# Performance work log

Measured on AMD Instinct MI355X. Metric: run time of the kernel, lower is better.

## Reference

```python
import jax, jax.numpy as jnp
import numpy as np

N_NODES = 50000
N_EDGES = 800000
D_IN, D_HID, D_OUT = 128, 128, 64


def setup_inputs() -> dict:
    key = jax.random.key(0)
    ks = jax.random.split(key, 10)
    return {
        "x": jax.random.normal(ks[0], (N_NODES, D_IN), dtype=jnp.float32),
        "edge_row": jax.random.randint(ks[1], (N_EDGES,), 0, N_NODES, dtype=jnp.int32),
        "edge_col": jax.random.randint(ks[2], (N_EDGES,), 0, N_NODES, dtype=jnp.int32),
        "edge_val": jax.random.uniform(ks[3], (N_EDGES,), dtype=jnp.float32),
        "W1": jax.random.normal(ks[4], (D_IN, D_HID), dtype=jnp.float32) * (1.0 / np.sqrt(D_HID)),
        "b1": jax.random.normal(ks[5], (D_HID,), dtype=jnp.float32) * (1.0 / np.sqrt(D_HID)),
        "W2": jax.random.normal(ks[6], (D_HID, D_HID), dtype=jnp.float32) * (1.0 / np.sqrt(D_HID)),
        "b2": jax.random.normal(ks[7], (D_HID,), dtype=jnp.float32) * (1.0 / np.sqrt(D_HID)),
        "W3": jax.random.normal(ks[8], (D_HID, D_OUT), dtype=jnp.float32) * (1.0 / np.sqrt(D_OUT)),
        "b3": jax.random.normal(ks[9], (D_OUT,), dtype=jnp.float32) * (1.0 / np.sqrt(D_OUT)),
    }


def _gcn_layer(x, edge_row, edge_col, edge_val, W, b):
    # support = x @ W          : dense GEMM [N, d_out]
    support = x @ W
    # spmm(adj, support)[i] = sum_e with row[e]==i: val[e] * support[col[e]]
    gathered = support[edge_col] * edge_val[:, None]  # [E, d_out]
    agg = jax.ops.segment_sum(gathered, edge_row, num_segments=x.shape[0])
    return agg + b


def reference(x, edge_row, edge_col, edge_val, W1, b1, W2, b2, W3, b3):
    # Layer 1 + ReLU (dropout is identity in eval)
    h = jax.nn.relu(_gcn_layer(x, edge_row, edge_col, edge_val, W1, b1))
    # Layer 2 + ReLU
    h = jax.nn.relu(_gcn_layer(h, edge_row, edge_col, edge_val, W2, b2))
    # Layer 3 (no activation)
    return _gcn_layer(h, edge_row, edge_col, edge_val, W3, b3)
```

## Files before the change

kernel.cpp:

```cpp
#include <hip/hip_runtime.h>

#define N_NODES 50000
#define N_EDGES 800000
#define SCAN_TILE 2048
#define CNT_STRIDE 16

static_assert(N_NODES < 65536, "col must fit in 16 bits for packed CSR");

typedef __attribute__((ext_vector_type(4))) float f32x4;
typedef __attribute__((ext_vector_type(8))) short bf16x8;

__device__ inline unsigned short f32_to_bf16(float f) {
    unsigned int u = __builtin_bit_cast(unsigned int, f);
    u += 0x7FFF + ((u >> 16) & 1);
    return (unsigned short)(u >> 16);
}
__device__ inline float bf16_to_f32(unsigned short h) {
    unsigned int u = ((unsigned int)h) << 16;
    return __builtin_bit_cast(float, u);
}

#define XN4   ((long long)N_NODES * 128 / 4)
#define W128  (128 * 128)
#define W64   (128 * 64)
#define CNT4  (N_NODES * CNT_STRIDE / 4)

__global__ void prep(const float* __restrict__ x, unsigned short* __restrict__ Xb,
                     const float* __restrict__ W1, const float* __restrict__ W2,
                     const float* __restrict__ W3, unsigned short* __restrict__ Wt1,
                     unsigned short* __restrict__ Wt2, unsigned short* __restrict__ Wt3,
                     int* __restrict__ cnt) {
    long long gid = (long long)blockIdx.x * blockDim.x + threadIdx.x;
    if (gid < XN4) {
        float4 v = reinterpret_cast<const float4*>(x)[gid];
        ushort4 o;
        o.x = f32_to_bf16(v.x); o.y = f32_to_bf16(v.y);
        o.z = f32_to_bf16(v.z); o.w = f32_to_bf16(v.w);
        reinterpret_cast<ushort4*>(Xb)[gid] = o;
        return;
    }
    long long r = gid - XN4;
    if (r < W128) {
        int k = (int)r / 128, m = (int)r % 128;
        Wt1[m * 128 + k] = f32_to_bf16(W1[r]);
        return;
    }
    r -= W128;
    if (r < W128) {
        int k = (int)r / 128, m = (int)r % 128;
        Wt2[m * 128 + k] = f32_to_bf16(W2[r]);
        return;
    }
    r -= W128;
    if (r < W64) {
        int k = (int)r / 64, m = (int)r % 64;
        Wt3[m * 128 + k] = f32_to_bf16(W3[r]);
        return;
    }
    r -= W64;
    if (r < CNT4) {
        int4 z = {0, 0, 0, 0};
        reinterpret_cast<int4*>(cnt)[r] = z;
    }
}

__global__ void rank_histogram(const int* __restrict__ erow, int* __restrict__ cnt,
                               int* __restrict__ rank) {
    int e = blockIdx.x * blockDim.x + threadIdx.x;
    if (e < N_EDGES) rank[e] = atomicAdd(&cnt[(size_t)erow[e] * CNT_STRIDE], 1);
}

__global__ void scan_tiles(const int* __restrict__ cnt, int* __restrict__ local,
                           int* __restrict__ tsum, int n) {
    __shared__ int sums[256];
    const int t = threadIdx.x;
    const int base = blockIdx.x * SCAN_TILE + t * 8;
    int v[8];
    int s = 0;
#pragma unroll
    for (int i = 0; i < 8; ++i) {
        v[i] = (base + i < n) ? cnt[(size_t)(base + i) * CNT_STRIDE] : 0;
        s += v[i];
    }
    sums[t] = s;
    __syncthreads();
    for (int off = 1; off < 256; off <<= 1) {
        int x = (t >= off) ? sums[t - off] : 0;
        __syncthreads();
        sums[t] += x;
        __syncthreads();
    }
    int run = sums[t] - s;
#pragma unroll
    for (int i = 0; i < 8; ++i) {
        if (base + i < n) local[base + i] = run;
        run += v[i];
    }
    if (t == 255) tsum[blockIdx.x] = run;
}

__global__ void scan_finalize(const int* __restrict__ local,
                              const int* __restrict__ tsum, int ntiles,
                              int* __restrict__ rptr, int n) {
    __shared__ int off_s;
    const int b = blockIdx.x;
    if (threadIdx.x == 0) {
        int s = 0;
        for (int i = 0; i < b; ++i) s += tsum[i];
        off_s = s;
        if (b == 0) {
            int tot = 0;
            for (int i = 0; i < ntiles; ++i) tot += tsum[i];
            rptr[n] = tot;
        }
    }
    __syncthreads();
    const int off = off_s;
    const int base = b * SCAN_TILE + threadIdx.x * 8;
#pragma unroll
    for (int i = 0; i < 8; ++i) {
        int idx = base + i;
        if (idx < n) rptr[idx] = local[idx] + off;
    }
}

__global__ void fill_csr(const int* __restrict__ erow, const int* __restrict__ ecol,
                         const float* __restrict__ eval, const int* __restrict__ rptr,
                         const int* __restrict__ rank,
                         unsigned int* __restrict__ cpack) {
    int e = blockIdx.x * blockDim.x + threadIdx.x;
    if (e >= N_EDGES) return;
    int slot = rptr[erow[e]] + rank[e];
    unsigned int p = (unsigned int)(ecol[e] & 0xFFFF) |
                     ((unsigned int)f32_to_bf16(eval[e]) << 16);
    cpack[slot] = p;
}

template <int NOUT, bool OUT_BF16>
__global__ __launch_bounds__(256) void gemm_mfma(
    const unsigned short* __restrict__ Xb, const unsigned short* __restrict__ Wt,
    void* __restrict__ Yv, int N, int ntiles) {
    constexpr int K = 128;
    constexpr int KP = K + 8;
    constexpr int NT = NOUT / 16;
    __shared__ unsigned short Xs[64 * KP];
    __shared__ unsigned short Ws[NOUT * KP];

    const int tid = threadIdx.x;
    const int wave = tid >> 6;
    const int lane = tid & 63;
    const int m = lane & 15;
    const int quad = lane >> 4;
    const int rowbase = wave * 16;

    for (int idx = tid; idx < NOUT * 16; idx += 256) {
        int r = idx >> 4, ch = idx & 15;
        uint4 v = *reinterpret_cast<const uint4*>(Wt + r * K + ch * 8);
        *reinterpret_cast<uint4*>(Ws + r * KP + ch * 8) = v;
    }

    for (int tile = blockIdx.x; tile < ntiles; tile += gridDim.x) {
        const int block_row = tile * 64;
        for (int idx = tid; idx < 64 * 16; idx += 256) {
            int r = idx >> 4, ch = idx & 15;
            int gr = block_row + r;
            if (gr >= N) gr = N - 1;
            uint4 v = *reinterpret_cast<const uint4*>(Xb + (size_t)gr * K + ch * 8);
            *reinterpret_cast<uint4*>(Xs + r * KP + ch * 8) = v;
        }
        __syncthreads();

        f32x4 acc[NT];
#pragma unroll
        for (int t = 0; t < NT; ++t) acc[t] = (f32x4){0.f, 0.f, 0.f, 0.f};

#pragma unroll
        for (int kt = 0; kt < 4; ++kt) {
            bf16x8 a = *reinterpret_cast<const bf16x8*>(
                Xs + (rowbase + m) * KP + kt * 32 + quad * 8);
#pragma unroll
            for (int t = 0; t < NT; ++t) {
                bf16x8 b = *reinterpret_cast<const bf16x8*>(
                    Ws + (t * 16 + m) * KP + kt * 32 + quad * 8);
                acc[t] = __builtin_amdgcn_mfma_f32_16x16x32_bf16(a, b, acc[t], 0, 0, 0);
            }
        }
        __syncthreads();

#pragma unroll
        for (int t = 0; t < NT; ++t) {
#pragma unroll
            for (int r = 0; r < 4; ++r) {
                int grow = block_row + rowbase + quad * 4 + r;
                if (grow < N) {
                    if (OUT_BF16)
                        reinterpret_cast<unsigned short*>(Yv)[(size_t)grow * NOUT + t * 16 + m] =
                            f32_to_bf16(acc[t][r]);
                    else
                        reinterpret_cast<float*>(Yv)[(size_t)grow * NOUT + t * 16 + m] = acc[t][r];
                }
            }
        }
    }
}

__global__ void aggregate_bf16(const unsigned short* __restrict__ S,
                               const int* __restrict__ rptr,
                               const unsigned int* __restrict__ cpack,
                               const float* __restrict__ bias,
                               unsigned short* __restrict__ outb, int N) {
    const int node = blockIdx.x * (blockDim.x / 16) + threadIdx.x / 16;
    const int f8 = threadIdx.x & 15;
    if (node >= N) return;
    const int beg = rptr[node];
    const int end = rptr[node + 1];
    float acc[8];
#pragma unroll
    for (int i = 0; i < 8; ++i) acc[i] = bias[f8 * 8 + i];
    int j = beg;
    for (; j + 8 <= end; j += 8) {
        unsigned int p[8];
        uint4 s[8];
#pragma unroll
        for (int u = 0; u < 8; ++u) p[u] = cpack[j + u];
#pragma unroll
        for (int u = 0; u < 8; ++u)
            s[u] = *reinterpret_cast<const uint4*>(S + (size_t)(p[u] & 0xFFFF) * 128 + f8 * 8);
#pragma unroll
        for (int u = 0; u < 8; ++u) {
            const float v = bf16_to_f32((unsigned short)(p[u] >> 16));
            const unsigned short* sp = reinterpret_cast<const unsigned short*>(&s[u]);
#pragma unroll
            for (int i = 0; i < 8; ++i) acc[i] = fmaf(v, bf16_to_f32(sp[i]), acc[i]);
        }
    }
    if (j + 4 <= end) {
        unsigned int p[4];
        uint4 s[4];
#pragma unroll
        for (int u = 0; u < 4; ++u) p[u] = cpack[j + u];
#pragma unroll
        for (int u = 0; u < 4; ++u)
            s[u] = *reinterpret_cast<const uint4*>(S + (size_t)(p[u] & 0xFFFF) * 128 + f8 * 8);
#pragma unroll
        for (int u = 0; u < 4; ++u) {
            const float v = bf16_to_f32((unsigned short)(p[u] >> 16));
            const unsigned short* sp = reinterpret_cast<const unsigned short*>(&s[u]);
#pragma unroll
            for (int i = 0; i < 8; ++i) acc[i] = fmaf(v, bf16_to_f32(sp[i]), acc[i]);
        }
        j += 4;
    }
    if (j + 2 <= end) {
        unsigned int p[2];
        uint4 s[2];
#pragma unroll
        for (int u = 0; u < 2; ++u) p[u] = cpack[j + u];
#pragma unroll
        for (int u = 0; u < 2; ++u)
            s[u] = *reinterpret_cast<const uint4*>(S + (size_t)(p[u] & 0xFFFF) * 128 + f8 * 8);
#pragma unroll
        for (int u = 0; u < 2; ++u) {
            const float v = bf16_to_f32((unsigned short)(p[u] >> 16));
            const unsigned short* sp = reinterpret_cast<const unsigned short*>(&s[u]);
#pragma unroll
            for (int i = 0; i < 8; ++i) acc[i] = fmaf(v, bf16_to_f32(sp[i]), acc[i]);
        }
        j += 2;
    }
    if (j < end) {
        unsigned int p = cpack[j];
        uint4 s = *reinterpret_cast<const uint4*>(S + (size_t)(p & 0xFFFF) * 128 + f8 * 8);
        const float v = bf16_to_f32((unsigned short)(p >> 16));
        const unsigned short* sp = reinterpret_cast<const unsigned short*>(&s);
#pragma unroll
        for (int i = 0; i < 8; ++i) acc[i] = fmaf(v, bf16_to_f32(sp[i]), acc[i]);
    }
    unsigned short o[8];
#pragma unroll
    for (int i = 0; i < 8; ++i) o[i] = f32_to_bf16(fmaxf(acc[i], 0.0f));
    *reinterpret_cast<uint4*>(outb + (size_t)node * 128 + f8 * 8) =
        *reinterpret_cast<uint4*>(o);
}

__global__ void aggregate_bf16_64(const unsigned short* __restrict__ S,
                                  const int* __restrict__ rptr,
                                  const unsigned int* __restrict__ cpack,
                                  const float* __restrict__ bias,
                                  float* __restrict__ out, int N) {
    const int node = blockIdx.x * (blockDim.x / 16) + threadIdx.x / 16;
    const int f4 = threadIdx.x & 15;
    if (node >= N) return;
    const int beg = rptr[node];
    const int end = rptr[node + 1];
    float acc[4];
#pragma unroll
    for (int i = 0; i < 4; ++i) acc[i] = bias[f4 * 4 + i];
    int j = beg;
    for (; j + 8 <= end; j += 8) {
        unsigned int p[8];
        uint2 s[8];
#pragma unroll
        for (int u = 0; u < 8; ++u) p[u] = cpack[j + u];
#pragma unroll
        for (int u = 0; u < 8; ++u)
            s[u] = *reinterpret_cast<const uint2*>(S + (size_t)(p[u] & 0xFFFF) * 64 + f4 * 4);
#pragma unroll
        for (int u = 0; u < 8; ++u) {
            const float v = bf16_to_f32((unsigned short)(p[u] >> 16));
            const unsigned short* sp = reinterpret_cast<const unsigned short*>(&s[u]);
#pragma unroll
            for (int i = 0; i < 4; ++i) acc[i] = fmaf(v, bf16_to_f32(sp[i]), acc[i]);
        }
    }
    if (j + 4 <= end) {
        unsigned int p[4];
        uint2 s[4];
#pragma unroll
        for (int u = 0; u < 4; ++u) p[u] = cpack[j + u];
#pragma unroll
        for (int u = 0; u < 4; ++u)
            s[u] = *reinterpret_cast<const uint2*>(S + (size_t)(p[u] & 0xFFFF) * 64 + f4 * 4);
#pragma unroll
        for (int u = 0; u < 4; ++u) {
            const float v = bf16_to_f32((unsigned short)(p[u] >> 16));
            const unsigned short* sp = reinterpret_cast<const unsigned short*>(&s[u]);
#pragma unroll
            for (int i = 0; i < 4; ++i) acc[i] = fmaf(v, bf16_to_f32(sp[i]), acc[i]);
        }
        j += 4;
    }
    if (j + 2 <= end) {
        unsigned int p[2];
        uint2 s[2];
#pragma unroll
        for (int u = 0; u < 2; ++u) p[u] = cpack[j + u];
#pragma unroll
        for (int u = 0; u < 2; ++u)
            s[u] = *reinterpret_cast<const uint2*>(S + (size_t)(p[u] & 0xFFFF) * 64 + f4 * 4);
#pragma unroll
        for (int u = 0; u < 2; ++u) {
            const float v = bf16_to_f32((unsigned short)(p[u] >> 16));
            const unsigned short* sp = reinterpret_cast<const unsigned short*>(&s[u]);
#pragma unroll
            for (int i = 0; i < 4; ++i) acc[i] = fmaf(v, bf16_to_f32(sp[i]), acc[i]);
        }
        j += 2;
    }
    if (j < end) {
        unsigned int p = cpack[j];
        uint2 s = *reinterpret_cast<const uint2*>(S + (size_t)(p & 0xFFFF) * 64 + f4 * 4);
        const float v = bf16_to_f32((unsigned short)(p >> 16));
        const unsigned short* sp = reinterpret_cast<const unsigned short*>(&s);
#pragma unroll
        for (int i = 0; i < 4; ++i) acc[i] = fmaf(v, bf16_to_f32(sp[i]), acc[i]);
    }
    float4 o = {acc[0], acc[1], acc[2], acc[3]};
    *reinterpret_cast<float4*>(out + (size_t)node * 64 + f4 * 4) = o;
}

extern "C" void kernel_launch(void* const* d_in, const int* in_sizes, int n_in,
                              void* d_out, int out_size, void* d_ws, size_t ws_size,
                              hipStream_t stream) {
    const float* x    = (const float*)d_in[0];
    const int*   erow = (const int*)d_in[1];
    const int*   ecol = (const int*)d_in[2];
    const float* eval = (const float*)d_in[3];
    const float* W1   = (const float*)d_in[4];
    const float* b1   = (const float*)d_in[5];
    const float* W2   = (const float*)d_in[6];
    const float* b2   = (const float*)d_in[7];
    const float* W3   = (const float*)d_in[8];
    const float* b3   = (const float*)d_in[9];
    float* out = (float*)d_out;

    const size_t nf = (size_t)N_NODES * 128;
    unsigned short* Xb  = (unsigned short*)d_ws;
    unsigned short* Ab  = Xb + nf;
    unsigned short* Wt1 = Ab + nf;
    unsigned short* Wt2 = Wt1 + 128 * 128;
    unsigned short* Wt3 = Wt2 + 128 * 128;
    int*   cnt    = (int*)(Wt3 + 64 * 128);
    int*   rank   = cnt + (size_t)N_NODES * CNT_STRIDE;
    int*   rptr   = rank + N_EDGES;
    unsigned int* cpack = (unsigned int*)(rptr + N_NODES + 1);
    int*   slocal = (int*)(cpack + N_EDGES);
    int*   stsum  = slocal + N_NODES;

    const int blk = 256;
    const int ntiles_g = (N_NODES + 63) / 64;
    const int gemm_grid = 256;
    const int agg_grid = (int)(((long long)N_NODES * 16 + blk - 1) / blk);
    const int ntiles = (N_NODES + SCAN_TILE - 1) / SCAN_TILE;

    {
        long long total = XN4 + W128 + W128 + W64 + CNT4;
        prep<<<(int)((total + blk - 1) / blk), blk, 0, stream>>>(
            x, Xb, W1, W2, W3, Wt1, Wt2, Wt3, cnt);
    }
    rank_histogram<<<(N_EDGES + blk - 1) / blk, blk, 0, stream>>>(erow, cnt, rank);
    scan_tiles<<<ntiles, 256, 0, stream>>>(cnt, slocal, stsum, N_NODES);
    scan_finalize<<<ntiles, 256, 0, stream>>>(slocal, stsum, ntiles, rptr, N_NODES);
    fill_csr<<<(N_EDGES + blk - 1) / blk, blk, 0, stream>>>(erow, ecol, eval, rptr,
                                                            rank, cpack);

    gemm_mfma<128, true><<<gemm_grid, 256, 0, stream>>>(Xb, Wt1, Ab, N_NODES, ntiles_g);
    aggregate_bf16<<<agg_grid, blk, 0, stream>>>(Ab, rptr, cpack, b1, Xb, N_NODES);

    gemm_mfma<128, true><<<gemm_grid, 256, 0, stream>>>(Xb, Wt2, Ab, N_NODES, ntiles_g);
    aggregate_bf16<<<agg_grid, blk, 0, stream>>>(Ab, rptr, cpack, b2, Xb, N_NODES);

    gemm_mfma<64, true><<<gemm_grid, 256, 0, stream>>>(Xb, Wt3, Ab, N_NODES, ntiles_g);
    aggregate_bf16_64<<<agg_grid, blk, 0, stream>>>(Ab, rptr, cpack, b3, out, N_NODES);
}
```

Measured before the change: 271.4 us.

## Fuse input conversion into GEMM1, merge scan kernels, overlap CSR fill with GEMM1

The first GEMM now reads the fp32 input directly and converts it to bf16 while staging into shared memory. This removes the separate pass that wrote and re-read a bf16 copy of x. The two scan kernels become one, with blocks coordinating through an atomic counter and spin-wait, which relies on all scan blocks being resident at once. The CSR fill runs as extra blocks inside the GEMM1 launch. Together these cut kernel launches and a full-size memory round trip.

```diff
diff --git a/kernel.cpp b/kernel.cpp
--- a/kernel.cpp
+++ b/kernel.cpp
@@ -4,6 +4,7 @@
 #define N_EDGES 800000
 #define SCAN_TILE 2048
 #define CNT_STRIDE 16
+#define GEMM_BLOCKS 256
 
 static_assert(N_NODES < 65536, "col must fit in 16 bits for packed CSR");
 
@@ -20,26 +21,16 @@
     return __builtin_bit_cast(float, u);
 }
 
-#define XN4   ((long long)N_NODES * 128 / 4)
 #define W128  (128 * 128)
 #define W64   (128 * 64)
 #define CNT4  (N_NODES * CNT_STRIDE / 4)
 
-__global__ void prep(const float* __restrict__ x, unsigned short* __restrict__ Xb,
-                     const float* __restrict__ W1, const float* __restrict__ W2,
+__global__ void prep(const float* __restrict__ W1, const float* __restrict__ W2,
                      const float* __restrict__ W3, unsigned short* __restrict__ Wt1,
                      unsigned short* __restrict__ Wt2, unsigned short* __restrict__ Wt3,
                      int* __restrict__ cnt) {
     long long gid = (long long)blockIdx.x * blockDim.x + threadIdx.x;
-    if (gid < XN4) {
-        float4 v = reinterpret_cast<const float4*>(x)[gid];
-        ushort4 o;
-        o.x = f32_to_bf16(v.x); o.y = f32_to_bf16(v.y);
-        o.z = f32_to_bf16(v.z); o.w = f32_to_bf16(v.w);
-        reinterpret_cast<ushort4*>(Xb)[gid] = o;
-        return;
-    }
-    long long r = gid - XN4;
+    long long r = gid;
     if (r < W128) {
         int k = (int)r / 128, m = (int)r % 128;
         Wt1[m * 128 + k] = f32_to_bf16(W1[r]);
@@ -70,12 +61,15 @@
     if (e < N_EDGES) rank[e] = atomicAdd(&cnt[(size_t)erow[e] * CNT_STRIDE], 1);
 }
 
-__global__ void scan_tiles(const int* __restrict__ cnt, int* __restrict__ local,
-                           int* __restrict__ tsum, int n) {
+__global__ void scan_fused(const int* __restrict__ cnt, int* __restrict__ tsum,
+                           int* __restrict__ done, int* __restrict__ rptr,
+                           int n, int ntiles) {
     __shared__ int sums[256];
+    __shared__ int off_s;
     const int t = threadIdx.x;
-    const int base = blockIdx.x * SCAN_TILE + t * 8;
-    int v[8];
+    const int b = blockIdx.x;
+    const int base = b * SCAN_TILE + t * 8;
+    int v[8], pref[8];
     int s = 0;
 #pragma unroll
     for (int i = 0; i < 8; ++i) {
@@ -93,21 +87,22 @@
     int run = sums[t] - s;
 #pragma unroll
     for (int i = 0; i < 8; ++i) {
-        if (base + i < n) local[base + i] = run;
+        pref[i] = run;
         run += v[i];
     }
-    if (t == 255) tsum[blockIdx.x] = run;
-}
-
-__global__ void scan_finalize(const int* __restrict__ local,
-                              const int* __restrict__ tsum, int ntiles,
-                              int* __restrict__ rptr, int n) {
-    __shared__ int off_s;
-    const int b = blockIdx.x;
-    if (threadIdx.x == 0) {
-        int s = 0;
-        for (int i = 0; i < b; ++i) s += tsum[i];
-        off_s = s;
+    if (t == 255) {
+        tsum[b] = run;
+        __threadfence();
+        atomicAdd(done, 1);
+    }
+    if (t == 0) {
+        while (__hip_atomic_load(done, __ATOMIC_ACQUIRE, __HIP_MEMORY_SCOPE_AGENT) <
+               ntiles) {
+        }
+        __threadfence();
+        int off = 0;
+        for (int i = 0; i < b; ++i) off += tsum[i];
+        off_s = off;
         if (b == 0) {
             int tot = 0;
             for (int i = 0; i < ntiles; ++i) tot += tsum[i];
@@ -116,35 +111,21 @@
     }
     __syncthreads();
     const int off = off_s;
-    const int base = b * SCAN_TILE + threadIdx.x * 8;
 #pragma unroll
     for (int i = 0; i < 8; ++i) {
         int idx = base + i;
-        if (idx < n) rptr[idx] = local[idx] + off;
-    }
-}
-
-__global__ void fill_csr(const int* __restrict__ erow, const int* __restrict__ ecol,
-                         const float* __restrict__ eval, const int* __restrict__ rptr,
-                         const int* __restrict__ rank,
-                         unsigned int* __restrict__ cpack) {
-    int e = blockIdx.x * blockDim.x + threadIdx.x;
-    if (e >= N_EDGES) return;
-    int slot = rptr[erow[e]] + rank[e];
-    unsigned int p = (unsigned int)(ecol[e] & 0xFFFF) |
-                     ((unsigned int)f32_to_bf16(eval[e]) << 16);
-    cpack[slot] = p;
-}
-
-template <int NOUT, bool OUT_BF16>
-__global__ __launch_bounds__(256) void gemm_mfma(
-    const unsigned short* __restrict__ Xb, const unsigned short* __restrict__ Wt,
-    void* __restrict__ Yv, int N, int ntiles) {
+        if (idx < n) rptr[idx] = pref[i] + off;
+    }
+}
+
+template <int NOUT, bool OUT_BF16, bool IN_F32>
+__device__ __forceinline__ void gemm_body(
+    const void* __restrict__ Xin, const unsigned short* __restrict__ Wt,
+    void* __restrict__ Yv, int N, int ntiles, int bid, int nblocks,
+    unsigned short* Xs, unsigned short* Ws) {
     constexpr int K = 128;
     constexpr int KP = K + 8;
     constexpr int NT = NOUT / 16;
-    __shared__ unsigned short Xs[64 * KP];
-    __shared__ unsigned short Ws[NOUT * KP];
 
     const int tid = threadIdx.x;
     const int wave = tid >> 6;
@@ -159,14 +140,33 @@
         *reinterpret_cast<uint4*>(Ws + r * KP + ch * 8) = v;
     }
 
-    for (int tile = blockIdx.x; tile < ntiles; tile += gridDim.x) {
+    for (int tile = bid; tile < ntiles; tile += nblocks) {
         const int block_row = tile * 64;
-        for (int idx = tid; idx < 64 * 16; idx += 256) {
-            int r = idx >> 4, ch = idx & 15;
-            int gr = block_row + r;
-            if (gr >= N) gr = N - 1;
-            uint4 v = *reinterpret_cast<const uint4*>(Xb + (size_t)gr * K + ch * 8);
-            *reinterpret_cast<uint4*>(Xs + r * KP + ch * 8) = v;
+        if (IN_F32) {
+            const float* xf = (const float*)Xin;
+            for (int idx = tid; idx < 64 * 16; idx += 256) {
+                int r = idx >> 4, ch = idx & 15;
+                int gr = block_row + r;
+                if (gr >= N) gr = N - 1;
+                const float4* xp =
+                    reinterpret_cast<const float4*>(xf + (size_t)gr * K + ch * 8);
+                float4 a = xp[0], b = xp[1];
+                uint4 o;
+                o.x = (unsigned int)f32_to_bf16(a.x) | ((unsigned int)f32_to_bf16(a.y) << 16);
+                o.y = (unsigned int)f32_to_bf16(a.z) | ((unsigned int)f32_to_bf16(a.w) << 16);
+                o.z = (unsigned int)f32_to_bf16(b.x) | ((unsigned int)f32_to_bf16(b.y) << 16);
+                o.w = (unsigned int)f32_to_bf16(b.z) | ((unsigned int)f32_to_bf16(b.w) << 16);
+                *reinterpret_cast<uint4*>(Xs + r * KP + ch * 8) = o;
+            }
+        } else {
+            const unsigned short* xb = (const unsigned short*)Xin;
+            for (int idx = tid; idx < 64 * 16; idx += 256) {
+                int r = idx >> 4, ch = idx & 15;
+                int gr = block_row + r;
+                if (gr >= N) gr = N - 1;
+                uint4 v = *reinterpret_cast<const uint4*>(xb + (size_t)gr * K + ch * 8);
+                *reinterpret_cast<uint4*>(Xs + r * KP + ch * 8) = v;
+            }
         }
         __syncthreads();
 
@@ -200,6 +200,40 @@
                         reinterpret_cast<float*>(Yv)[(size_t)grow * NOUT + t * 16 + m] = acc[t][r];
                 }
             }
+        }
+    }
+}
+
+template <int NOUT, bool OUT_BF16>
+__global__ __launch_bounds__(256) void gemm_mfma(
+    const unsigned short* __restrict__ Xb, const unsigned short* __restrict__ Wt,
+    void* __restrict__ Yv, int N, int ntiles) {
+    constexpr int KP = 128 + 8;
+    __shared__ unsigned short Xs[64 * KP];
+    __shared__ unsigned short Ws[NOUT * KP];
+    gemm_body<NOUT, OUT_BF16, false>(Xb, Wt, Yv, N, ntiles, blockIdx.x, gridDim.x,
+                                     Xs, Ws);
+}
+
+__global__ __launch_bounds__(256) void gemm1_fill(
+    const float* __restrict__ x, const unsigned short* __restrict__ Wt,
+    unsigned short* __restrict__ Yb, int N, int ntiles,
+    const int* __restrict__ erow, const int* __restrict__ ecol,
+    const float* __restrict__ eval, const int* __restrict__ rptr,
+    const int* __restrict__ rank, unsigned int* __restrict__ cpack) {
+    constexpr int KP = 128 + 8;
+    __shared__ unsigned short Xs[64 * KP];
+    __shared__ unsigned short Ws[128 * KP];
+    if (blockIdx.x < GEMM_BLOCKS) {
+        gemm_body<128, true, true>(x, Wt, Yb, N, ntiles, blockIdx.x, GEMM_BLOCKS,
+                                   Xs, Ws);
+    } else {
+        int e = (blockIdx.x - GEMM_BLOCKS) * blockDim.x + threadIdx.x;
+        if (e < N_EDGES) {
+            int slot = rptr[erow[e]] + rank[e];
+            unsigned int p = (unsigned int)(ecol[e] & 0xFFFF) |
+                             ((unsigned int)f32_to_bf16(eval[e]) << 16);
+            cpack[slot] = p;
         }
     }
 }
@@ -384,32 +418,30 @@
     int*   rank   = cnt + (size_t)N_NODES * CNT_STRIDE;
     int*   rptr   = rank + N_EDGES;
     unsigned int* cpack = (unsigned int*)(rptr + N_NODES + 1);
-    int*   slocal = (int*)(cpack + N_EDGES);
-    int*   stsum  = slocal + N_NODES;
+    int*   stsum  = (int*)(cpack + N_EDGES);
+    int*   done   = cnt + 1;
 
     const int blk = 256;
     const int ntiles_g = (N_NODES + 63) / 64;
-    const int gemm_grid = 256;
     const int agg_grid = (int)(((long long)N_NODES * 16 + blk - 1) / blk);
     const int ntiles = (N_NODES + SCAN_TILE - 1) / SCAN_TILE;
+    const int fill_blocks = (N_EDGES + blk - 1) / blk;
 
     {
-        long long total = XN4 + W128 + W128 + W64 + CNT4;
+        long long total = W128 + W128 + W64 + CNT4;
         prep<<<(int)((total + blk - 1) / blk), blk, 0, stream>>>(
-            x, Xb, W1, W2, W3, Wt1, Wt2, Wt3, cnt);
+            W1, W2, W3, Wt1, Wt2, Wt3, cnt);
     }
     rank_histogram<<<(N_EDGES + blk - 1) / blk, blk, 0, stream>>>(erow, cnt, rank);
-    scan_tiles<<<ntiles, 256, 0, stream>>>(cnt, slocal, stsum, N_NODES);
-    scan_finalize<<<ntiles, 256, 0, stream>>>(slocal, stsum, ntiles, rptr, N_NODES);
-    fill_csr<<<(N_EDGES + blk - 1) / blk, blk, 0, stream>>>(erow, ecol, eval, rptr,
-                                                            rank, cpack);
-
-    gemm_mfma<128, true><<<gemm_grid, 256, 0, stream>>>(Xb, Wt1, Ab, N_NODES, ntiles_g);
+    scan_fused<<<ntiles, 256, 0, stream>>>(cnt, stsum, done, rptr, N_NODES, ntiles);
+
+    gemm1_fill<<<GEMM_BLOCKS + fill_blocks, 256, 0, stream>>>(
+        x, Wt1, Ab, N_NODES, ntiles_g, erow, ecol, eval, rptr, rank, cpack);
     aggregate_bf16<<<agg_grid, blk, 0, stream>>>(Ab, rptr, cpack, b1, Xb, N_NODES);
 
-    gemm_mfma<128, true><<<gemm_grid, 256, 0, stream>>>(Xb, Wt2, Ab, N_NODES, ntiles_g);
+    gemm_mfma<128, true><<<GEMM_BLOCKS, 256, 0, stream>>>(Xb, Wt2, Ab, N_NODES, ntiles_g);
     aggregate_bf16<<<agg_grid, blk, 0, stream>>>(Ab, rptr, cpack, b2, Xb, N_NODES);
 
-    gemm_mfma<64, true><<<gemm_grid, 256, 0, stream>>>(Xb, Wt3, Ab, N_NODES, ntiles_g);
+    gemm_mfma<64, true><<<GEMM_BLOCKS, 256, 0, stream>>>(Xb, Wt3, Ab, N_NODES, ntiles_g);
     aggregate_bf16_64<<<agg_grid, blk, 0, stream>>>(Ab, rptr, cpack, b3, out, N_NODES);
 }
```

After: 262.8 us. 1.03x faster.
